# Optimization experiments

Hardware: AMD Instinct MI355X
Metric: run time of the kernel (lower is better)

## Reference

```python
import jax, jax.numpy as jnp
import numpy as np

B, T, D, L = 16, 4096, 512, 1024

def setup_inputs() -> dict:
    key = jax.random.key(0)
    k1, k2, k3, k4 = jax.random.split(key, 4)
    x = jax.random.normal(k1, (B, T, D), dtype=jnp.float32)
    q = jax.random.normal(k2, (L, D), dtype=jnp.float32)
    fc_w = jax.random.normal(k3, (1, D), dtype=jnp.float32) * (1.0 / np.sqrt(D))
    fc_b = jax.random.normal(k4, (1,), dtype=jnp.float32) * 0.01
    return {"x": x, "q": q, "fc_w": fc_w, "fc_b": fc_b}

def reference(x, q, fc_w, fc_b):
    # att: (B, T, L) label-wise attention scores, softmax over sequence axis T
    att = jnp.einsum('btd,ld->btl', x, q)
    att = jax.nn.softmax(att, axis=1)
    # out: (B, L, D) attention-pooled features per label
    out = jnp.einsum('btl,btd->bld', att, x)
    # linear head to scalar per label -> (B, L)
    return jnp.einsum('bld,od->blo', out, fc_w).squeeze(-1) + fc_b[0]
```

## Files before the change

### kernel.cpp

```cpp
#include <hip/hip_runtime.h>

#define B_ 16
#define T_ 4096
#define D_ 512
#define L_ 1024
#define NTCH 32
#define PPLANE ((size_t)B_ * NTCH * L_)

typedef _Float16 half8 __attribute__((ext_vector_type(8)));
typedef _Float16 h4_t  __attribute__((ext_vector_type(4)));
typedef float float4v __attribute__((ext_vector_type(4)));

__device__ inline void gl_lds(const void* g, void* l) {
    __builtin_amdgcn_global_load_lds(
        (const __attribute__((address_space(1))) unsigned int*)g,
        (__attribute__((address_space(3))) unsigned int*)l, 16, 0, 0);
}

__global__ __launch_bounds__(256) void k_y(const float* __restrict__ x,
                                           const float* __restrict__ w,
                                           float* __restrict__ y) {
    int row  = blockIdx.x * 4 + (threadIdx.x >> 6);
    int lane = threadIdx.x & 63;
    const float4* r = (const float4*)(x + (size_t)row * D_);
    const float4* wv = (const float4*)w;
    float4 a = r[lane], b = r[lane + 64];
    float4 wa = wv[lane], wb = wv[lane + 64];
    float s = a.x * wa.x;
    s = fmaf(a.y, wa.y, s); s = fmaf(a.z, wa.z, s); s = fmaf(a.w, wa.w, s);
    s = fmaf(b.x, wb.x, s); s = fmaf(b.y, wb.y, s);
    s = fmaf(b.z, wb.z, s); s = fmaf(b.w, wb.w, s);
#pragma unroll
    for (int o = 32; o > 0; o >>= 1) s += __shfl_xor(s, o, 64);
    if (lane == 0) y[row] = s;
}

__global__ __launch_bounds__(256) void k_qcvt(const float* __restrict__ src,
                                              _Float16* __restrict__ dst) {
    int idx = blockIdx.x * 256 + threadIdx.x;
    int g   = idx & 63;
    int row = idx >> 6;
    const float* p = src + (size_t)row * D_ + g * 8;
    float4 a = *(const float4*)p;
    float4 c = *(const float4*)(p + 4);
    half8 h;
    h[0] = (_Float16)a.x; h[1] = (_Float16)a.y; h[2] = (_Float16)a.z; h[3] = (_Float16)a.w;
    h[4] = (_Float16)c.x; h[5] = (_Float16)c.y; h[6] = (_Float16)c.z; h[7] = (_Float16)c.w;
    size_t blk = (size_t)(row >> 4) * (D_ / 32) + (g >> 2);
    ((half8*)dst)[blk * 64 + (row & 15) + 16 * (g & 3)] = h;
}

__global__ __launch_bounds__(256, 2) void k_mfma(const float* __restrict__ x,
                                                 const _Float16* __restrict__ qt,
                                                 const float* __restrict__ y,
                                                 float* __restrict__ part) {
    __shared__ _Float16 Sx[256 * 72];
    __shared__ half8 Sq[1024];
    __shared__ float ys[256];

    const int bid  = blockIdx.x;
    const int xcd  = bid & 7;
    const int jj   = bid >> 3;
    const int tile = (xcd << 5) | (jj >> 3);
    const int lblk = jj & 7;
    const int tblk = tile & 15;
    const int b    = tile >> 4;

    const int tid  = threadIdx.x;
    const int lane = tid & 63;
    const int w    = tid >> 6;
    const int wt   = w >> 1, wl = w & 1;
    const int rq   = lane >> 4, ch = lane & 15;
    const int lb0  = lblk * 8;

    ys[tid] = y[(size_t)b * T_ + tblk * 256 + tid];

    float4v acc[8][4];
#pragma unroll
    for (int i = 0; i < 8; ++i)
#pragma unroll
        for (int j = 0; j < 4; ++j) acc[i][j] = (float4v){0.f, 0.f, 0.f, 0.f};

    const half8* Qg = (const half8*)qt;
    const float* xb = x + ((size_t)b * T_ + tblk * 256) * D_;

    for (int kk = 0; kk < D_ / 64; ++kk) {
        __syncthreads();
#pragma unroll
        for (int p = 0; p < 4; ++p) {
            int u = p * 4 + w;
            gl_lds(Qg + ((size_t)(lb0 + (u & 7)) * (D_ / 32) + kk * 2 + (u >> 3)) * 64 + lane,
                   &Sq[u * 64]);
        }
#pragma unroll
        for (int it = 0; it < 16; ++it) {
            int row = w * 64 + it * 4 + rq;
            float4 a = *(const float4*)(xb + (size_t)row * D_ + kk * 64 + ch * 4);
            h4_t h = {(_Float16)a.x, (_Float16)a.y, (_Float16)a.z, (_Float16)a.w};
            *(h4_t*)&Sx[row * 72 + ch * 4] = h;
        }
        __syncthreads();

#pragma unroll
        for (int s = 0; s < 2; ++s) {
            half8 A[8], Bv[4];
#pragma unroll
            for (int i = 0; i < 8; ++i)
                A[i] = *(const half8*)&Sx[(wt * 128 + i * 16 + ch) * 72 + s * 32 + rq * 8];
#pragma unroll
            for (int j = 0; j < 4; ++j)
                Bv[j] = Sq[((u_int32_t)s * 8 + wl * 4 + j) * 64 + lane];
#pragma unroll
            for (int i = 0; i < 8; ++i)
#pragma unroll
                for (int j = 0; j < 4; ++j)
                    acc[i][j] = __builtin_amdgcn_mfma_f32_16x16x32_f16(A[i], Bv[j], acc[i][j], 0, 0, 0);
        }
    }

    const int quad = lane >> 4, cl = lane & 15;
    const int tchunk = tblk * 2 + wt;
    const int lbase  = lblk * 128 + wl * 64;

    float* pm = part;
    float* pz = part + PPLANE;
    float* pn = part + 2 * PPLANE;

#pragma unroll
    for (int j = 0; j < 4; ++j) {
        float m = -1e30f;
#pragma unroll
        for (int i = 0; i < 8; ++i)
#pragma unroll
            for (int r = 0; r < 4; ++r) m = fmaxf(m, acc[i][j][r]);
        float z = 0.f, n = 0.f;
#pragma unroll
        for (int i = 0; i < 8; ++i)
#pragma unroll
            for (int r = 0; r < 4; ++r) {
                float p = __expf(acc[i][j][r] - m);
                z += p;
                n = fmaf(p, ys[wt * 128 + i * 16 + quad * 4 + r], n);
            }
#pragma unroll
        for (int msk = 16; msk <= 32; msk <<= 1) {
            float om = __shfl_xor(m, msk, 64);
            float oz = __shfl_xor(z, msk, 64);
            float on = __shfl_xor(n, msk, 64);
            float mn = fmaxf(m, om);
            float s0 = __expf(m - mn), s1 = __expf(om - mn);
            z = fmaf(z, s0, oz * s1);
            n = fmaf(n, s0, on * s1);
            m = mn;
        }
        if (quad == 0) {
            int l = lbase + j * 16 + cl;
            size_t a = ((size_t)b * NTCH + tchunk) * L_ + l;
            pm[a] = m;
            pz[a] = z;
            pn[a] = n;
        }
    }
}

__global__ __launch_bounds__(256) void k_comb_p(const float* __restrict__ part,
                                                const float* __restrict__ fc_b,
                                                float* __restrict__ out) {
    int bl = blockIdx.x * 256 + threadIdx.x;
    int b = bl >> 10, l = bl & (L_ - 1);
    const float* pm = part;
    const float* pz = part + PPLANE;
    const float* pn = part + 2 * PPLANE;
    float m = -1e30f, z = 0.f, n = 0.f;
    for (int c = 0; c < NTCH; ++c) {
        size_t a = ((size_t)b * NTCH + c) * L_ + l;
        float pmv = pm[a], pzv = pz[a], pnv = pn[a];
        float mn = fmaxf(m, pmv);
        float s0 = __expf(m - mn), s1 = __expf(pmv - mn);
        z = fmaf(z, s0, pzv * s1);
        n = fmaf(n, s0, pnv * s1);
        m = mn;
    }
    out[bl] = n / z + fc_b[0];
}

#define NC 8
#define TC (T_ / NC)
#define BT 128
#define BL 128
#define KK 32

__global__ __launch_bounds__(256, 2) void k_main(const float* __restrict__ x,
                                                 const float* __restrict__ q,
                                                 const float* __restrict__ y,
                                                 float* __restrict__ part) {
    __shared__ float Xs[KK][BT + 4];
    __shared__ float Qs[KK][BL + 4];
    const int tid = threadIdx.x;
    const int ty = tid & 15, tx = tid >> 4;
    const int lb = blockIdx.x * BL, chunk = blockIdx.y, b = blockIdx.z;
    const int g = tid & 7, r0 = tid >> 3;

    float run_m[8], run_z[8], run_n[8];
#pragma unroll
    for (int j = 0; j < 8; ++j) { run_m[j] = -1e30f; run_z[j] = 0.f; run_n[j] = 0.f; }

    for (int tt = 0; tt < TC; tt += BT) {
        const int t0 = chunk * TC + tt;
        float s[8][8];
#pragma unroll
        for (int i = 0; i < 8; ++i)
#pragma unroll
            for (int j = 0; j < 8; ++j) s[i][j] = 0.f;
        for (int kc = 0; kc < D_; kc += KK) {
            __syncthreads();
#pragma unroll
            for (int p = 0; p < 4; ++p) {
                int rr = p * 32 + r0;
                float4 vx = *(const float4*)(x + ((size_t)b * T_ + t0 + rr) * D_ + kc + g * 4);
                float4 vq = *(const float4*)(q + (size_t)(lb + rr) * D_ + kc + g * 4);
                Xs[g * 4 + 0][rr] = vx.x; Xs[g * 4 + 1][rr] = vx.y;
                Xs[g * 4 + 2][rr] = vx.z; Xs[g * 4 + 3][rr] = vx.w;
                Qs[g * 4 + 0][rr] = vq.x; Qs[g * 4 + 1][rr] = vq.y;
                Qs[g * 4 + 2][rr] = vq.z; Qs[g * 4 + 3][rr] = vq.w;
            }
            __syncthreads();
#pragma unroll
            for (int k = 0; k < KK; ++k) {
                float4 a0 = *(const float4*)&Xs[k][ty * 4];
                float4 a1 = *(const float4*)&Xs[k][64 + ty * 4];
                float4 b0 = *(const float4*)&Qs[k][tx * 4];
                float4 b1 = *(const float4*)&Qs[k][64 + tx * 4];
                float av[8] = {a0.x, a0.y, a0.z, a0.w, a1.x, a1.y, a1.z, a1.w};
                float bv[8] = {b0.x, b0.y, b0.z, b0.w, b1.x, b1.y, b1.z, b1.w};
#pragma unroll
                for (int i = 0; i < 8; ++i)
#pragma unroll
                    for (int j = 0; j < 8; ++j) s[i][j] = fmaf(av[i], bv[j], s[i][j]);
            }
        }
        float yv[8];
#pragma unroll
        for (int i = 0; i < 8; ++i) {
            int tl = (i < 4) ? (ty * 4 + i) : (64 + ty * 4 + (i - 4));
            yv[i] = y[(size_t)b * T_ + t0 + tl];
        }
#pragma unroll
        for (int j = 0; j < 8; ++j) {
            float mt = s[0][j];
#pragma unroll
            for (int i = 1; i < 8; ++i) mt = fmaxf(mt, s[i][j]);
            float mn = fmaxf(run_m[j], mt);
            float sc = __expf(run_m[j] - mn);
            float z = run_z[j] * sc, n = run_n[j] * sc;
#pragma unroll
            for (int i = 0; i < 8; ++i) {
                float p = __expf(s[i][j] - mn);
                z += p;
                n = fmaf(p, yv[i], n);
            }
            run_m[j] = mn; run_z[j] = z; run_n[j] = n;
        }
    }
#pragma unroll
    for (int msk = 1; msk < 16; msk <<= 1) {
#pragma unroll
        for (int j = 0; j < 8; ++j) {
            float om = __shfl_xor(run_m[j], msk, 64);
            float oz = __shfl_xor(run_z[j], msk, 64);
            float on = __shfl_xor(run_n[j], msk, 64);
            float mn = fmaxf(run_m[j], om);
            float s0 = __expf(run_m[j] - mn), s1 = __expf(om - mn);
            run_z[j] = fmaf(run_z[j], s0, oz * s1);
            run_n[j] = fmaf(run_n[j], s0, on * s1);
            run_m[j] = mn;
        }
    }
    if (ty == 0) {
#pragma unroll
        for (int j = 0; j < 8; ++j) {
            int ll = (j < 4) ? (tx * 4 + j) : (64 + tx * 4 + (j - 4));
            size_t idx = ((size_t)(b * L_ + lb + ll) * NC + chunk) * 3;
            part[idx + 0] = run_m[j];
            part[idx + 1] = run_z[j];
            part[idx + 2] = run_n[j];
        }
    }
}

__global__ __launch_bounds__(256) void k_comb_f(const float* __restrict__ part,
                                                const float* __restrict__ fc_b,
                                                float* __restrict__ out) {
    int bl = blockIdx.x * 256 + threadIdx.x;
    float m = -1e30f, z = 0.f, n = 0.f;
    for (int c = 0; c < NC; ++c) {
        size_t idx = ((size_t)bl * NC + c) * 3;
        float pm = part[idx + 0], pz = part[idx + 1], pn = part[idx + 2];
        float mn = fmaxf(m, pm);
        float s0 = __expf(m - mn), s1 = __expf(pm - mn);
        z = fmaf(z, s0, pz * s1);
        n = fmaf(n, s0, pn * s1);
        m = mn;
    }
    out[bl] = n / z + fc_b[0];
}

extern "C" void kernel_launch(void* const* d_in, const int* in_sizes, int n_in,
                              void* d_out, int out_size, void* d_ws, size_t ws_size,
                              hipStream_t stream) {
    const float* x    = (const float*)d_in[0];
    const float* q    = (const float*)d_in[1];
    const float* fc_w = (const float*)d_in[2];
    const float* fc_b = (const float*)d_in[3];
    float* out = (float*)d_out;
    float* ws  = (float*)d_ws;

    const size_t Y_F    = (size_t)B_ * T_;
    const size_t PART_F = 3 * PPLANE;
    const size_t QT_H   = (size_t)L_ * D_;
    const size_t need   = (Y_F + PART_F) * 4 + QT_H * 2;

    if (ws_size >= need) {
        float* y    = ws;
        float* part = ws + Y_F;
        _Float16* qt = (_Float16*)(ws + Y_F + PART_F);
        k_y   <<<B_ * T_ / 4, 256, 0, stream>>>(x, fc_w, y);
        k_qcvt<<<(L_ * 64) / 256, 256, 0, stream>>>(q, qt);
        k_mfma<<<2048, 256, 0, stream>>>(x, qt, y, part);
        k_comb_p<<<B_ * L_ / 256, 256, 0, stream>>>(part, fc_b, out);
    } else {
        float* y    = ws;
        float* part = ws + Y_F;
        k_y   <<<B_ * T_ / 4, 256, 0, stream>>>(x, fc_w, y);
        k_main<<<dim3(L_ / BL, NC, B_), 256, 0, stream>>>(x, q, y, part);
        k_comb_f<<<B_ * L_ / 256, 256, 0, stream>>>(part, fc_b, out);
    }
}
```

Before: 285.4 us.

## Pre-convert x to fp16 in fused prep kernel and stream tiles via LDS DMA

Adds a fused prep kernel that computes the fc projection y, converts all of x to fp16 in a workspace buffer, and converts q to row-major fp16. The MFMA kernel then loads both x and q tiles with global_load_lds into XOR-swizzled LDS instead of doing per-iteration fp32 loads and register conversion. The aim is to halve x traffic inside the GEMM and drop conversion work from its inner loop. The cost is an extra full write and read of an fp16 copy of x (64 MB), plus a larger workspace requirement that may push execution onto the fallback path.

```diff
diff --git a/kernel.cpp b/kernel.cpp
--- a/kernel.cpp
+++ b/kernel.cpp
@@ -8,7 +8,6 @@
 #define PPLANE ((size_t)B_ * NTCH * L_)
 
 typedef _Float16 half8 __attribute__((ext_vector_type(8)));
-typedef _Float16 h4_t  __attribute__((ext_vector_type(4)));
 typedef float float4v __attribute__((ext_vector_type(4)));
 
 __device__ inline void gl_lds(const void* g, void* l) {
@@ -17,45 +16,44 @@
         (__attribute__((address_space(3))) unsigned int*)l, 16, 0, 0);
 }
 
-__global__ __launch_bounds__(256) void k_y(const float* __restrict__ x,
-                                           const float* __restrict__ w,
-                                           float* __restrict__ y) {
-    int row  = blockIdx.x * 4 + (threadIdx.x >> 6);
-    int lane = threadIdx.x & 63;
-    const float4* r = (const float4*)(x + (size_t)row * D_);
-    const float4* wv = (const float4*)w;
-    float4 a = r[lane], b = r[lane + 64];
-    float4 wa = wv[lane], wb = wv[lane + 64];
-    float s = a.x * wa.x;
-    s = fmaf(a.y, wa.y, s); s = fmaf(a.z, wa.z, s); s = fmaf(a.w, wa.w, s);
-    s = fmaf(b.x, wb.x, s); s = fmaf(b.y, wb.y, s);
-    s = fmaf(b.z, wb.z, s); s = fmaf(b.w, wb.w, s);
-#pragma unroll
-    for (int o = 32; o > 0; o >>= 1) s += __shfl_xor(s, o, 64);
-    if (lane == 0) y[row] = s;
-}
-
-__global__ __launch_bounds__(256) void k_qcvt(const float* __restrict__ src,
-                                              _Float16* __restrict__ dst) {
-    int idx = blockIdx.x * 256 + threadIdx.x;
-    int g   = idx & 63;
-    int row = idx >> 6;
-    const float* p = src + (size_t)row * D_ + g * 8;
-    float4 a = *(const float4*)p;
-    float4 c = *(const float4*)(p + 4);
+__global__ __launch_bounds__(256) void k_prep(const float* __restrict__ x,
+                                              const float* __restrict__ q,
+                                              const float* __restrict__ w,
+                                              _Float16* __restrict__ xt,
+                                              _Float16* __restrict__ qt,
+                                              float* __restrict__ y) {
+    int i = blockIdx.x * 256 + threadIdx.x;
+    int row = i >> 6, seg = i & 63;
+    bool isq = row >= B_ * T_;
+    const float* src = isq ? (q + (size_t)(row - B_ * T_) * D_)
+                           : (x + (size_t)row * D_);
+    _Float16* dst = isq ? (qt + (size_t)(row - B_ * T_) * D_)
+                        : (xt + (size_t)row * D_);
+    float4 a = *(const float4*)(src + seg * 8);
+    float4 c = *(const float4*)(src + seg * 8 + 4);
     half8 h;
     h[0] = (_Float16)a.x; h[1] = (_Float16)a.y; h[2] = (_Float16)a.z; h[3] = (_Float16)a.w;
     h[4] = (_Float16)c.x; h[5] = (_Float16)c.y; h[6] = (_Float16)c.z; h[7] = (_Float16)c.w;
-    size_t blk = (size_t)(row >> 4) * (D_ / 32) + (g >> 2);
-    ((half8*)dst)[blk * 64 + (row & 15) + 16 * (g & 3)] = h;
-}
-
-__global__ __launch_bounds__(256, 2) void k_mfma(const float* __restrict__ x,
+    *(half8*)(dst + seg * 8) = h;
+    if (!isq) {
+        float4 wa = *(const float4*)(w + seg * 8);
+        float4 wc = *(const float4*)(w + seg * 8 + 4);
+        float s = a.x * wa.x;
+        s = fmaf(a.y, wa.y, s); s = fmaf(a.z, wa.z, s); s = fmaf(a.w, wa.w, s);
+        s = fmaf(c.x, wc.x, s); s = fmaf(c.y, wc.y, s); s = fmaf(c.z, wc.z, s);
+        s = fmaf(c.w, wc.w, s);
+#pragma unroll
+        for (int o = 32; o > 0; o >>= 1) s += __shfl_xor(s, o, 64);
+        if (seg == 0) y[row] = s;
+    }
+}
+
+__global__ __launch_bounds__(256, 2) void k_mfma(const _Float16* __restrict__ xt,
                                                  const _Float16* __restrict__ qt,
                                                  const float* __restrict__ y,
                                                  float* __restrict__ part) {
-    __shared__ _Float16 Sx[256 * 72];
-    __shared__ half8 Sq[1024];
+    __shared__ _Float16 Sx[256 * 64];
+    __shared__ _Float16 Sq[128 * 64];
     __shared__ float ys[256];
 
     const int bid  = blockIdx.x;
@@ -70,8 +68,9 @@
     const int lane = tid & 63;
     const int w    = tid >> 6;
     const int wt   = w >> 1, wl = w & 1;
-    const int rq   = lane >> 4, ch = lane & 15;
-    const int lb0  = lblk * 8;
+    const int ch   = lane & 15, rq = lane >> 4;
+    const int srow = lane >> 3;
+    const int sgr  = (lane & 7) ^ srow;
 
     ys[tid] = y[(size_t)b * T_ + tblk * 256 + tid];
 
@@ -81,35 +80,35 @@
 #pragma unroll
         for (int j = 0; j < 4; ++j) acc[i][j] = (float4v){0.f, 0.f, 0.f, 0.f};
 
-    const half8* Qg = (const half8*)qt;
-    const float* xb = x + ((size_t)b * T_ + tblk * 256) * D_;
+    const _Float16* xb = xt + ((size_t)b * T_ + tblk * 256) * D_;
+    const _Float16* qb = qt + (size_t)lblk * 128 * D_;
 
     for (int kk = 0; kk < D_ / 64; ++kk) {
         __syncthreads();
 #pragma unroll
+        for (int p = 0; p < 8; ++p) {
+            int rg = p * 4 + w;
+            gl_lds(xb + (size_t)(rg * 8 + srow) * D_ + kk * 64 + sgr * 8,
+                   &Sx[rg * 512]);
+        }
+#pragma unroll
         for (int p = 0; p < 4; ++p) {
-            int u = p * 4 + w;
-            gl_lds(Qg + ((size_t)(lb0 + (u & 7)) * (D_ / 32) + kk * 2 + (u >> 3)) * 64 + lane,
-                   &Sq[u * 64]);
-        }
-#pragma unroll
-        for (int it = 0; it < 16; ++it) {
-            int row = w * 64 + it * 4 + rq;
-            float4 a = *(const float4*)(xb + (size_t)row * D_ + kk * 64 + ch * 4);
-            h4_t h = {(_Float16)a.x, (_Float16)a.y, (_Float16)a.z, (_Float16)a.w};
-            *(h4_t*)&Sx[row * 72 + ch * 4] = h;
+            int rg = p * 4 + w;
+            gl_lds(qb + (size_t)(rg * 8 + srow) * D_ + kk * 64 + sgr * 8,
+                   &Sq[rg * 512]);
         }
         __syncthreads();
 
 #pragma unroll
         for (int s = 0; s < 2; ++s) {
+            const int d = (s * 4 + rq) ^ (ch & 7);
             half8 A[8], Bv[4];
 #pragma unroll
             for (int i = 0; i < 8; ++i)
-                A[i] = *(const half8*)&Sx[(wt * 128 + i * 16 + ch) * 72 + s * 32 + rq * 8];
+                A[i] = *(const half8*)&Sx[(wt * 128 + i * 16 + ch) * 64 + d * 8];
 #pragma unroll
             for (int j = 0; j < 4; ++j)
-                Bv[j] = Sq[((u_int32_t)s * 8 + wl * 4 + j) * 64 + lane];
+                Bv[j] = *(const half8*)&Sq[(wl * 64 + j * 16 + ch) * 64 + d * 8];
 #pragma unroll
             for (int i = 0; i < 8; ++i)
 #pragma unroll
@@ -190,6 +189,20 @@
 #define BL 128
 #define KK 32
 
+__global__ __launch_bounds__(256) void k_y(const float* __restrict__ x,
+                                           const float* __restrict__ w,
+                                           float* __restrict__ y) {
+    int row  = (blockIdx.x * 256 + threadIdx.x) >> 6;
+    int lane = threadIdx.x & 63;
+    const float* r = x + (size_t)row * D_;
+    float s = 0.f;
+#pragma unroll
+    for (int k = 0; k < D_; k += 64) s = fmaf(r[k + lane], w[k + lane], s);
+#pragma unroll
+    for (int o = 32; o > 0; o >>= 1) s += __shfl_xor(s, o, 64);
+    if (lane == 0) y[row] = s;
+}
+
 __global__ __launch_bounds__(256, 2) void k_main(const float* __restrict__ x,
                                                  const float* __restrict__ q,
                                                  const float* __restrict__ y,
@@ -317,16 +330,17 @@
 
     const size_t Y_F    = (size_t)B_ * T_;
     const size_t PART_F = 3 * PPLANE;
+    const size_t XT_H   = (size_t)B_ * T_ * D_;
     const size_t QT_H   = (size_t)L_ * D_;
-    const size_t need   = (Y_F + PART_F) * 4 + QT_H * 2;
+    const size_t need   = (Y_F + PART_F) * 4 + (XT_H + QT_H) * 2;
 
     if (ws_size >= need) {
         float* y    = ws;
         float* part = ws + Y_F;
-        _Float16* qt = (_Float16*)(ws + Y_F + PART_F);
-        k_y   <<<B_ * T_ / 4, 256, 0, stream>>>(x, fc_w, y);
-        k_qcvt<<<(L_ * 64) / 256, 256, 0, stream>>>(q, qt);
-        k_mfma<<<2048, 256, 0, stream>>>(x, qt, y, part);
+        _Float16* xt = (_Float16*)(ws + Y_F + PART_F);
+        _Float16* qt = xt + XT_H;
+        k_prep<<<(B_ * T_ + L_) / 4, 256, 0, stream>>>(x, q, fc_w, xt, qt, y);
+        k_mfma<<<2048, 256, 0, stream>>>(xt, qt, y, part);
         k_comb_p<<<B_ * L_ / 256, 256, 0, stream>>>(part, fc_b, out);
     } else {
         float* y    = ws;
```

Result: faster. 270.4 us (-5.2%).
